# Kernel optimization log

Hardware: AMD Instinct MI355X
Metric: run time of the kernel (lower is better)

## Reference

```python
import jax, jax.numpy as jnp
import numpy as np

S, B, E, H = 512, 64, 512, 512  # seq_len, batch, embed_dim, lstm_dim


def setup_inputs() -> dict:
    key = jax.random.key(0)
    ks = jax.random.split(key, 16)
    scale = 0.03

    def W(k):
        return jax.random.normal(k, (E + H, H), jnp.float32) * scale

    return {
        "embedded_tokens": jax.random.normal(ks[0], (S, B, E), jnp.float32),
        "hidden0": jnp.zeros((B, H), jnp.float32),
        "context0": jnp.zeros((B, H), jnp.float32),
        "Wf": W(ks[1]), "bf": jnp.zeros((H,), jnp.float32),
        "Wi": W(ks[2]), "bi": jnp.zeros((H,), jnp.float32),
        "Wo": W(ks[3]), "bo": jnp.zeros((H,), jnp.float32),
        "Wc": W(ks[4]), "bc": jnp.zeros((H,), jnp.float32),
        "Wmf": W(ks[5]), "bmf": jnp.zeros((H,), jnp.float32),
        "Wmi": W(ks[6]), "bmi": jnp.zeros((H,), jnp.float32),
        "seq_lengths": jax.random.randint(ks[7], (B,), 1, S + 1, jnp.int32),
    }


def reference(embedded_tokens, hidden0, context0, Wf, bf, Wi, bi, Wo, bo,
              Wc, bc, Wmf, bmf, Wmi, bmi, seq_lengths):
    # ON-LSTM recurrence, dropout p=0.0 so dropout is identity.
    def step(carry, x_t):
        h, c = carry                                   # [B,H], [B,H]
        z = jnp.concatenate([x_t, h], axis=1)          # [B, E+H]
        ft = jax.nn.sigmoid(z @ Wf + bf)
        it = jax.nn.sigmoid(z @ Wi + bi)
        ot = jax.nn.sigmoid(z @ Wo + bo)
        c_hat = jnp.tanh(z @ Wc + bc)
        mf = jnp.cumsum(jax.nn.softmax(z @ Wmf + bmf, axis=1), axis=1)  # master forget (cumax)
        mi = jnp.cumsum(jax.nn.softmax(z @ Wmi + bmi, axis=1), axis=1)  # master input (cumax)
        wt = mf * mi
        f_hat = ft * wt + (mf - wt)
        i_hat = it * wt + (mi - wt)
        c = f_hat * c + i_hat * c_hat
        h = ot * c
        return (h, c), (h, c)

    (_h, _c), (all_h, all_c) = jax.lax.scan(step, (hidden0, context0), embedded_tokens)
    # gather final valid state per example
    t_idx = seq_lengths - 1                            # [B]
    b_idx = jnp.arange(all_h.shape[1])
    state_hidden = all_h[t_idx, b_idx]                 # [B,H]
    state_context = all_c[t_idx, b_idx]                # [B,H]
    return all_h, state_hidden, state_context
```

## Files before the change

kernel.cpp:

```cpp
#include <hip/hip_runtime.h>

#define S_LEN 512
#define NWG   64
#define COLS  48
#define OUT_ALLH (512*64*512)
#define OUT_SH   (OUT_ALLH)
#define OUT_SC   (OUT_ALLH + 64*512)

#define O_WT    0ull
#define SZ_WT   (3072ull*1024*2)
#define O_BIAS  (O_WT + SZ_WT)
#define SZ_BIAS (3072ull*4)
#define O_HBF   (O_BIAS + SZ_BIAS)
#define SZ_HBF  (2ull*64*512*2)
#define O_FLAGH (O_HBF + SZ_HBF)
#define O_FLAGP (O_FLAGH + 256)
#define O_P     (O_FLAGP + 256)
#define SZ_P    (64ull*128*4)
#define O_XBF   (O_P + SZ_P)
#define SZ_XBF  (512ull*64*512*2)
#define WS_FULL (O_XBF + SZ_XBF)

#define L_WLDS  0
#define L_PLDS  98304
#define L_GATES 132096
#define L_CST   145664
#define L_BLDS  147968
#define L_SLEN  148160
#define L_PART  148416
#define SMEM_TOTAL 150464

#define GSTR 53
#define PSTR 132

typedef short bf16x8 __attribute__((ext_vector_type(8)));
typedef float f32x4  __attribute__((ext_vector_type(4)));

__device__ __forceinline__ unsigned short f2bf(float f) {
  unsigned u = __float_as_uint(f);
  u += 0x7fffu + ((u >> 16) & 1u);
  return (unsigned short)(u >> 16);
}

#define ATOM_LD(p)    __hip_atomic_load((p), __ATOMIC_RELAXED, __HIP_MEMORY_SCOPE_AGENT)
#define ATOM_ST(p, v) __hip_atomic_store((p), (v), __ATOMIC_RELAXED, __HIP_MEMORY_SCOPE_AGENT)

struct PrepArgs {
  const float* W[6]; const float* bia[6];
  const float* h0;
  unsigned short* WT; float* bias_all; unsigned short* Hbf;
  int* flagH; int* flagP;
};

__global__ void prep_kernel(PrepArgs a) {
  const int n = blockIdx.x, tid = threadIdx.x;
  if (n < 3072) {
    const int q = n >> 9, col = n & 511;
    const float* Wq = a.W[q];
    for (int k = tid; k < 1024; k += 256)
      a.WT[(size_t)n*1024 + k] = f2bf(Wq[k*512 + col]);
    if (tid == 0) a.bias_all[n] = a.bia[q][col];
  } else if (n < 3136) {
    const int r = n - 3072;
    for (int h = tid; h < 512; h += 256) {
      const int w = h >> 3, c = h & 7;
      a.Hbf[(size_t)(64 + w)*512 + r*8 + c] = f2bf(a.h0[r*512 + h]);
    }
  } else {
    if (tid < 64) a.flagH[tid] = 0;
    else if (tid < 128) a.flagP[tid - 64] = 0;
  }
}

__global__ void convx_kernel(const float* __restrict__ x, unsigned short* __restrict__ xbf) {
  const size_t i = ((size_t)blockIdx.x*256 + threadIdx.x) * 4;
  float4 v = *(const float4*)(x + i);
  ushort4 r;
  r.x = f2bf(v.x); r.y = f2bf(v.y); r.z = f2bf(v.z); r.w = f2bf(v.w);
  *(ushort4*)(xbf + i) = r;
}

struct LstmArgs {
  const float* x; const unsigned short* xbf; const float* c0; const int* slen;
  const unsigned short* WT; const float* bias_all; unsigned short* Hbf;
  int* flagH; int* flagP; float* P; float* out;
};

__device__ __forceinline__ void gemm_q(const uint4* af, const char* wlds,
                                       int lane, int kh, f32x4* acc) {
  #pragma unroll
  for (int kt = 0; kt < 8; ++kt) {
    bf16x8 a = *(const bf16x8*)&af[kt];
    #pragma unroll
    for (int nt = 0; nt < 3; ++nt) {
      const int bcol = nt*16 + (lane & 15);
      const int bkc  = kh*32 + kt*4 + (lane >> 4);
      bf16x8 b = *(const bf16x8*)(wlds + bcol*2048 + (((bkc + bcol) & 127) << 4));
      acc[nt] = __builtin_amdgcn_mfma_f32_16x16x32_bf16(a, b, acc[nt], 0, 0, 0);
    }
  }
}

__device__ __forceinline__ void load_xf(const LstmArgs& a, bool ux, int t, int q,
                                        int arow, int lane, uint4 xf[8]) {
  #pragma unroll
  for (int kt = 0; kt < 8; ++kt) {
    const size_t off = ((size_t)t*64 + arow)*512 + (size_t)(q*32 + kt*4 + (lane >> 4))*8;
    if (ux) {
      xf[kt] = *(const uint4*)(a.xbf + off);
    } else {
      const float* sp = a.x + off;
      float4 v0 = *(const float4*)(sp);
      float4 v1 = *(const float4*)(sp + 4);
      xf[kt].x = (unsigned)f2bf(v0.x) | ((unsigned)f2bf(v0.y) << 16);
      xf[kt].y = (unsigned)f2bf(v0.z) | ((unsigned)f2bf(v0.w) << 16);
      xf[kt].z = (unsigned)f2bf(v1.x) | ((unsigned)f2bf(v1.y) << 16);
      xf[kt].w = (unsigned)f2bf(v1.z) | ((unsigned)f2bf(v1.w) << 16);
    }
  }
}

__launch_bounds__(256, 1)
__global__ void lstm_kernel(LstmArgs a) {
  extern __shared__ char smem[];
  char*  wlds  = smem + L_WLDS;
  float* Plds  = (float*)(smem + L_PLDS);
  float* gates = (float*)(smem + L_GATES);
  float* cst   = (float*)(smem + L_CST);
  float* blds  = (float*)(smem + L_BLDS);
  int*   slenl = (int*)(smem + L_SLEN);
  float* part  = (float*)(smem + L_PART);

  const int wg = blockIdx.x, tid = threadIdx.x;
  const int lane = tid & 63, wv = tid >> 6;
  const int arow = wv*16 + (lane & 15);
  const bool ux = (a.xbf != nullptr);

  for (int m = tid; m < COLS*128; m += 256) {
    const int col = m >> 7, kc = m & 127;
    const int q = col >> 3, c = col & 7;
    uint4 v = *(const uint4*)(a.WT + ((size_t)(q*512 + wg*8 + c))*1024 + kc*8);
    *(uint4*)(wlds + col*2048 + (((kc + col) & 127) << 4)) = v;
  }
  if (tid < COLS) { const int q = tid >> 3, c = tid & 7; blds[tid] = a.bias_all[q*512 + wg*8 + c]; }
  if (tid < 64) slenl[tid] = a.slen[tid];
  for (int e = tid; e < 512; e += 256) { const int r = e >> 3, c = e & 7; cst[r*9 + c] = a.c0[r*512 + wg*8 + c]; }
  __syncthreads();

  f32x4 accC[3] = { f32x4{0,0,0,0}, f32x4{0,0,0,0}, f32x4{0,0,0,0} };
  {
    uint4 xf[8];
    load_xf(a, ux, 0, 0, arow, lane, xf);
    gemm_q(xf, wlds, lane, 0, accC);
    load_xf(a, ux, 0, 1, arow, lane, xf);
    gemm_q(xf, wlds, lane, 1, accC);
  }

  for (int t = 0; t < S_LEN; ++t) {
    if (tid < 64) {
      while (ATOM_LD(&a.flagH[tid]) < t)
        __builtin_amdgcn_s_sleep(1);
    }
    __syncthreads();

    const int buf = (t+1) & 1;
    {
      uint4 hf[16];
      #pragma unroll
      for (int j = 0; j < 16; ++j) {
        const int wl = (j & 7)*4 + (lane >> 4) + ((j >> 3) << 5);
        const unsigned short* src = a.Hbf + ((size_t)(buf*64 + wl))*512 + (size_t)arow*8;
        asm volatile("global_load_dwordx4 %0, %1, off sc0 sc1" : "=v"(hf[j]) : "v"(src));
      }
      asm volatile("s_waitcnt vmcnt(8)" ::: "memory");
      __builtin_amdgcn_sched_barrier(0);
      gemm_q(&hf[0], wlds, lane, 2, accC);
      asm volatile("s_waitcnt vmcnt(0)" ::: "memory");
      __builtin_amdgcn_sched_barrier(0);
      gemm_q(&hf[8], wlds, lane, 3, accC);
    }

    #pragma unroll
    for (int nt = 0; nt < 3; ++nt)
      #pragma unroll
      for (int ri = 0; ri < 4; ++ri) {
        const int row = wv*16 + (lane >> 4)*4 + ri;
        gates[row*GSTR + nt*16 + (lane & 15)] = accC[nt][ri];
      }
    __syncthreads();

    const unsigned ep = (unsigned)(t & 1);
    const int tn = t + 1;

    if (tid < 128) {
      const int gi = tid >> 6, r = tid & 63;
      float s = 0.f;
      #pragma unroll
      for (int c = 0; c < 8; ++c) {
        float e = __expf(gates[r*GSTR + (4+gi)*8 + c] + blds[(4+gi)*8 + c]);
        gates[r*GSTR + (4+gi)*8 + c] = e;
        s += e;
      }
      ATOM_ST((unsigned*)(a.P + (size_t)wg*128 + tid), __float_as_uint(s) | (ep << 31));
    }

    f32x4 accN[3] = { f32x4{0,0,0,0}, f32x4{0,0,0,0}, f32x4{0,0,0,0} };
    uint4 xf[8];
    if (tn < S_LEN) {
      load_xf(a, ux, tn, 0, arow, lane, xf);
      gemm_q(xf, wlds, lane, 0, accN);
    }

    #pragma unroll
    for (int j = 0; j < 8; ++j) {
      const int m2 = tid + j*256;
      const int r = m2 >> 5, c = m2 & 31;
      const float v = gates[r*GSTR + c] + blds[c];
      const float e = __expf((c < 24) ? -v : 2.f*v);
      gates[r*GSTR + c] = (c < 24) ? 1.f/(1.f+e) : (e-1.f)/(e+1.f);
    }

    uint4 pbuf[8];
    {
      bool ok = false;
      do {
        #pragma unroll
        for (int j = 0; j < 8; ++j) {
          const int idx = tid + j*256;
          const float* src = a.P + (size_t)idx*4;
          asm volatile("global_load_dwordx4 %0, %1, off sc0 sc1" : "=v"(pbuf[j]) : "v"(src));
        }
        asm volatile("s_waitcnt vmcnt(0)" ::: "memory");
        __builtin_amdgcn_sched_barrier(0);
        unsigned agg = ep ? 0xFFFFFFFFu : 0u;
        #pragma unroll
        for (int j = 0; j < 8; ++j) {
          if (ep) agg &= (pbuf[j].x & pbuf[j].y & pbuf[j].z & pbuf[j].w);
          else    agg |= (pbuf[j].x | pbuf[j].y | pbuf[j].z | pbuf[j].w);
        }
        ok = ((agg >> 31) == ep);
        if (!ok) __builtin_amdgcn_s_sleep(1);
      } while (!ok);
    }

    #pragma unroll
    for (int j = 0; j < 8; ++j) {
      const int idx = tid + j*256;
      const int w = idx >> 5, o = (idx & 31)*4;
      *(uint4*)((char*)Plds + ((size_t)w*PSTR + o)*4) = pbuf[j];
    }
    __syncthreads();

    {
      const int p = tid >> 1, half = tid & 1;
      const int gi = p >> 6, r = p & 63;
      float tot = 0.f, offv = 0.f;
      #pragma unroll
      for (int i = 0; i < 32; ++i) {
        const int w = half*32 + i;
        const float v = __builtin_fabsf(Plds[w*PSTR + gi*64 + r]);
        tot += v;
        if (w < wg) offv += v;
      }
      *(float2*)(part + tid*2) = make_float2(tot, offv);
    }
    __syncthreads();
    if (tid < 128) {
      const int gi = tid >> 6, r = tid & 63;
      float4 pp = *(const float4*)(part + tid*4);
      const float inv = 1.f / (pp.x + pp.z);
      float run = pp.y + pp.w;
      #pragma unroll
      for (int c = 0; c < 8; ++c) {
        run += gates[r*GSTR + (4+gi)*8 + c];
        gates[r*GSTR + (4+gi)*8 + c] = run * inv;
      }
    }
    __syncthreads();

    float hv[2], cv2[2];
    const int er = tid >> 2, ec0 = (tid & 3)*2;
    {
      const float* g = gates + er*GSTR;
      #pragma unroll
      for (int u = 0; u < 2; ++u) {
        const int c = ec0 + u;
        const float ft = g[c];
        const float it = g[8 + c];
        const float ot = g[16 + c];
        const float ch = g[24 + c];
        const float mf = g[32 + c];
        const float mi = g[40 + c];
        const float w2 = mf * mi;
        const float fh = ft * w2 + (mf - w2);
        const float ih = it * w2 + (mi - w2);
        const float cn = fh * cst[er*9 + c] + ih * ch;
        cst[er*9 + c] = cn;
        cv2[u] = cn;
        hv[u] = ot * cn;
      }
      const unsigned pk = (unsigned)f2bf(hv[0]) | ((unsigned)f2bf(hv[1]) << 16);
      ATOM_ST((unsigned*)(a.Hbf + ((size_t)((t & 1)*64 + wg))*512 + er*8 + ec0), pk);
    }
    asm volatile("s_waitcnt vmcnt(0)" ::: "memory");
    __syncthreads();
    if (tid == 0) ATOM_ST(&a.flagH[wg], t+1);

    if (tn < S_LEN) {
      load_xf(a, ux, tn, 1, arow, lane, xf);
      gemm_q(xf, wlds, lane, 1, accN);
    }

    {
      const int col = wg*8 + ec0;
      *(float2*)(a.out + (size_t)t*32768 + er*512 + col) = make_float2(hv[0], hv[1]);
      if (t == slenl[er] - 1) {
        *(float2*)(a.out + (size_t)OUT_SH + er*512 + col) = make_float2(hv[0], hv[1]);
        *(float2*)(a.out + (size_t)OUT_SC + er*512 + col) = make_float2(cv2[0], cv2[1]);
      }
    }

    accC[0] = accN[0]; accC[1] = accN[1]; accC[2] = accN[2];
  }
}

extern "C" void kernel_launch(void* const* d_in, const int* in_sizes, int n_in,
                              void* d_out, int out_size, void* d_ws, size_t ws_size,
                              hipStream_t stream) {
  char* ws = (char*)d_ws;

  PrepArgs pa;
  for (int q = 0; q < 6; ++q) {
    pa.W[q]   = (const float*)d_in[3 + 2*q];
    pa.bia[q] = (const float*)d_in[4 + 2*q];
  }
  pa.h0       = (const float*)d_in[1];
  pa.WT       = (unsigned short*)(ws + O_WT);
  pa.bias_all = (float*)(ws + O_BIAS);
  pa.Hbf      = (unsigned short*)(ws + O_HBF);
  pa.flagH    = (int*)(ws + O_FLAGH);
  pa.flagP    = (int*)(ws + O_FLAGP);
  prep_kernel<<<3137, 256, 0, stream>>>(pa);

  const bool ux = (ws_size >= WS_FULL);
  if (ux)
    convx_kernel<<<16384, 256, 0, stream>>>((const float*)d_in[0], (unsigned short*)(ws + O_XBF));

  LstmArgs la;
  la.x        = (const float*)d_in[0];
  la.xbf      = ux ? (const unsigned short*)(ws + O_XBF) : nullptr;
  la.c0       = (const float*)d_in[2];
  la.slen     = (const int*)d_in[15];
  la.WT       = pa.WT;
  la.bias_all = pa.bias_all;
  la.Hbf      = pa.Hbf;
  la.flagH    = pa.flagH;
  la.flagP    = pa.flagP;
  la.P        = (float*)(ws + O_P);
  la.out      = (float*)d_out;

  hipFuncSetAttribute(reinterpret_cast<const void*>(lstm_kernel),
                      hipFuncAttributeMaxDynamicSharedMemorySize, SMEM_TOTAL);
  lstm_kernel<<<NWG, 256, SMEM_TOTAL, stream>>>(la);
}
```

Before: 4.047 ms.

## Embed step tags in hidden-state words, drop flag barrier, reorder gate GEMMs

Each bf16 hidden pair is now packed into a 64-bit word together with its timestep tag. Consumers poll the data itself until every tag matches, which replaces the separate per-workgroup flag, the store drain and the extra barrier. The hidden-state GEMM is reordered so the master-gate columns are computed first and their softmax partial sums are published early, before the other gate columns. This aims to shorten the per-step cross-workgroup critical path, at the cost of doubling hidden-state traffic and spinning on wider loads; the sleep in the partial-sum poll is also removed.

```diff
diff --git a/kernel.cpp b/kernel.cpp
--- a/kernel.cpp
+++ b/kernel.cpp
@@ -12,10 +12,8 @@
 #define O_BIAS  (O_WT + SZ_WT)
 #define SZ_BIAS (3072ull*4)
 #define O_HBF   (O_BIAS + SZ_BIAS)
-#define SZ_HBF  (2ull*64*512*2)
-#define O_FLAGH (O_HBF + SZ_HBF)
-#define O_FLAGP (O_FLAGH + 256)
-#define O_P     (O_FLAGP + 256)
+#define SZ_HBF  (2ull*64*64*4*8)
+#define O_P     (O_HBF + SZ_HBF)
 #define SZ_P    (64ull*128*4)
 #define O_XBF   (O_P + SZ_P)
 #define SZ_XBF  (512ull*64*512*2)
@@ -48,8 +46,7 @@
 struct PrepArgs {
   const float* W[6]; const float* bia[6];
   const float* h0;
-  unsigned short* WT; float* bias_all; unsigned short* Hbf;
-  int* flagH; int* flagP;
+  unsigned short* WT; float* bias_all; unsigned long long* Hbf;
 };
 
 __global__ void prep_kernel(PrepArgs a) {
@@ -60,15 +57,13 @@
     for (int k = tid; k < 1024; k += 256)
       a.WT[(size_t)n*1024 + k] = f2bf(Wq[k*512 + col]);
     if (tid == 0) a.bias_all[n] = a.bia[q][col];
-  } else if (n < 3136) {
+  } else {
     const int r = n - 3072;
-    for (int h = tid; h < 512; h += 256) {
-      const int w = h >> 3, c = h & 7;
-      a.Hbf[(size_t)(64 + w)*512 + r*8 + c] = f2bf(a.h0[r*512 + h]);
-    }
-  } else {
-    if (tid < 64) a.flagH[tid] = 0;
-    else if (tid < 128) a.flagP[tid - 64] = 0;
+    const int w = tid >> 2, u = tid & 3;
+    const int c0 = w*8 + u*2;
+    const unsigned pk = (unsigned)f2bf(a.h0[r*512 + c0]) |
+                        ((unsigned)f2bf(a.h0[r*512 + c0 + 1]) << 16);
+    a.Hbf[((size_t)(64 + w)*64 + r)*4 + u] = (unsigned long long)pk;
   }
 }
 
@@ -82,22 +77,25 @@
 
 struct LstmArgs {
   const float* x; const unsigned short* xbf; const float* c0; const int* slen;
-  const unsigned short* WT; const float* bias_all; unsigned short* Hbf;
-  int* flagH; int* flagP; float* P; float* out;
+  const unsigned short* WT; const float* bias_all; unsigned long long* Hbf;
+  float* P; float* out;
 };
 
-__device__ __forceinline__ void gemm_q(const uint4* af, const char* wlds,
-                                       int lane, int kh, f32x4* acc) {
+__device__ __forceinline__ void gemm_one(const uint4& afr, const char* wlds,
+                                         int lane, int bkc, int nt, f32x4& acc) {
+  const int bcol = nt*16 + (lane & 15);
+  bf16x8 b = *(const bf16x8*)(wlds + bcol*2048 + (((bkc + bcol) & 127) << 4));
+  bf16x8 av = *(const bf16x8*)&afr;
+  acc = __builtin_amdgcn_mfma_f32_16x16x32_bf16(av, b, acc, 0, 0, 0);
+}
+
+__device__ __forceinline__ void gemm_q3(const uint4* af, const char* wlds,
+                                        int lane, int kh, f32x4* acc) {
   #pragma unroll
   for (int kt = 0; kt < 8; ++kt) {
-    bf16x8 a = *(const bf16x8*)&af[kt];
-    #pragma unroll
-    for (int nt = 0; nt < 3; ++nt) {
-      const int bcol = nt*16 + (lane & 15);
-      const int bkc  = kh*32 + kt*4 + (lane >> 4);
-      bf16x8 b = *(const bf16x8*)(wlds + bcol*2048 + (((bkc + bcol) & 127) << 4));
-      acc[nt] = __builtin_amdgcn_mfma_f32_16x16x32_bf16(a, b, acc[nt], 0, 0, 0);
-    }
+    const int bkc = kh*32 + kt*4 + (lane >> 4);
+    #pragma unroll
+    for (int nt = 0; nt < 3; ++nt) gemm_one(af[kt], wlds, lane, bkc, nt, acc[nt]);
   }
 }
 
@@ -151,65 +149,96 @@
   {
     uint4 xf[8];
     load_xf(a, ux, 0, 0, arow, lane, xf);
-    gemm_q(xf, wlds, lane, 0, accC);
+    gemm_q3(xf, wlds, lane, 0, accC);
     load_xf(a, ux, 0, 1, arow, lane, xf);
-    gemm_q(xf, wlds, lane, 1, accC);
+    gemm_q3(xf, wlds, lane, 1, accC);
   }
 
   for (int t = 0; t < S_LEN; ++t) {
-    if (tid < 64) {
-      while (ATOM_LD(&a.flagH[tid]) < t)
-        __builtin_amdgcn_s_sleep(1);
-    }
-    __syncthreads();
-
     const int buf = (t+1) & 1;
-    {
-      uint4 hf[16];
-      #pragma unroll
-      for (int j = 0; j < 16; ++j) {
-        const int wl = (j & 7)*4 + (lane >> 4) + ((j >> 3) << 5);
-        const unsigned short* src = a.Hbf + ((size_t)(buf*64 + wl))*512 + (size_t)arow*8;
-        asm volatile("global_load_dwordx4 %0, %1, off sc0 sc1" : "=v"(hf[j]) : "v"(src));
-      }
-      asm volatile("s_waitcnt vmcnt(8)" ::: "memory");
-      __builtin_amdgcn_sched_barrier(0);
-      gemm_q(&hf[0], wlds, lane, 2, accC);
-      asm volatile("s_waitcnt vmcnt(0)" ::: "memory");
-      __builtin_amdgcn_sched_barrier(0);
-      gemm_q(&hf[8], wlds, lane, 3, accC);
-    }
-
-    #pragma unroll
-    for (int nt = 0; nt < 3; ++nt)
+    const unsigned expect = (unsigned)t;
+    const unsigned long long* Hq = a.Hbf + (size_t)buf*16384;
+
+    uint4 hf[16];
+    #pragma unroll
+    for (int q = 0; q < 2; ++q) {
+      bool ok;
+      do {
+        uint4 raw[16];
+        #pragma unroll
+        for (int kt = 0; kt < 8; ++kt) {
+          const int c8 = q*32 + kt*4 + (lane >> 4);
+          const unsigned long long* up = Hq + (size_t)c8*256 + (size_t)arow*4;
+          asm volatile("global_load_dwordx4 %0, %1, off sc0 sc1" : "=v"(raw[kt*2])   : "v"(up));
+          asm volatile("global_load_dwordx4 %0, %1, off sc0 sc1" : "=v"(raw[kt*2+1]) : "v"(up+2));
+        }
+        asm volatile("s_waitcnt vmcnt(0)" ::: "memory");
+        __builtin_amdgcn_sched_barrier(0);
+        unsigned diff = 0;
+        #pragma unroll
+        for (int kt = 0; kt < 8; ++kt) {
+          const uint4 r0 = raw[kt*2], r1 = raw[kt*2+1];
+          hf[q*8+kt] = uint4{r0.x, r0.z, r1.x, r1.z};
+          diff |= (r0.y ^ expect) | (r0.w ^ expect) | (r1.y ^ expect) | (r1.w ^ expect);
+        }
+        ok = (diff == 0u);
+        if (!ok) __builtin_amdgcn_s_sleep(1);
+      } while (!ok);
+    }
+
+    #pragma unroll
+    for (int q = 0; q < 2; ++q)
+      #pragma unroll
+      for (int kt = 0; kt < 8; ++kt)
+        gemm_one(hf[q*8+kt], wlds, lane, (2+q)*32 + kt*4 + (lane >> 4), 2, accC[2]);
+
+    #pragma unroll
+    for (int ri = 0; ri < 4; ++ri) {
+      const int row = wv*16 + (lane >> 4)*4 + ri;
+      gates[row*GSTR + 32 + (lane & 15)] = accC[2][ri];
+    }
+    __syncthreads();
+
+    const unsigned ep = (unsigned)(t & 1);
+    const int tn = t + 1;
+
+    if (tid < 128) {
+      const int gi = tid >> 6, r = tid & 63;
+      float s = 0.f;
+      #pragma unroll
+      for (int c = 0; c < 8; ++c) {
+        float e = __expf(gates[r*GSTR + 32 + gi*8 + c] + blds[32 + gi*8 + c]);
+        e = fmaxf(e, 1e-30f);
+        gates[r*GSTR + 32 + gi*8 + c] = e;
+        s += e;
+      }
+      ATOM_ST((unsigned*)(a.P + (size_t)wg*128 + tid), __float_as_uint(s) | (ep << 31));
+    }
+
+    #pragma unroll
+    for (int q = 0; q < 2; ++q)
+      #pragma unroll
+      for (int kt = 0; kt < 8; ++kt) {
+        const int bkc = (2+q)*32 + kt*4 + (lane >> 4);
+        gemm_one(hf[q*8+kt], wlds, lane, bkc, 0, accC[0]);
+        gemm_one(hf[q*8+kt], wlds, lane, bkc, 1, accC[1]);
+      }
+
+    #pragma unroll
+    for (int nt = 0; nt < 2; ++nt)
       #pragma unroll
       for (int ri = 0; ri < 4; ++ri) {
         const int row = wv*16 + (lane >> 4)*4 + ri;
         gates[row*GSTR + nt*16 + (lane & 15)] = accC[nt][ri];
       }
-    __syncthreads();
-
-    const unsigned ep = (unsigned)(t & 1);
-    const int tn = t + 1;
-
-    if (tid < 128) {
-      const int gi = tid >> 6, r = tid & 63;
-      float s = 0.f;
-      #pragma unroll
-      for (int c = 0; c < 8; ++c) {
-        float e = __expf(gates[r*GSTR + (4+gi)*8 + c] + blds[(4+gi)*8 + c]);
-        gates[r*GSTR + (4+gi)*8 + c] = e;
-        s += e;
-      }
-      ATOM_ST((unsigned*)(a.P + (size_t)wg*128 + tid), __float_as_uint(s) | (ep << 31));
-    }
 
     f32x4 accN[3] = { f32x4{0,0,0,0}, f32x4{0,0,0,0}, f32x4{0,0,0,0} };
     uint4 xf[8];
     if (tn < S_LEN) {
       load_xf(a, ux, tn, 0, arow, lane, xf);
-      gemm_q(xf, wlds, lane, 0, accN);
-    }
+      gemm_q3(xf, wlds, lane, 0, accN);
+    }
+    __syncthreads();
 
     #pragma unroll
     for (int j = 0; j < 8; ++j) {
@@ -239,7 +268,6 @@
           else    agg |= (pbuf[j].x | pbuf[j].y | pbuf[j].z | pbuf[j].w);
         }
         ok = ((agg >> 31) == ep);
-        if (!ok) __builtin_amdgcn_s_sleep(1);
       } while (!ok);
     }
 
@@ -272,14 +300,14 @@
       float run = pp.y + pp.w;
       #pragma unroll
       for (int c = 0; c < 8; ++c) {
-        run += gates[r*GSTR + (4+gi)*8 + c];
-        gates[r*GSTR + (4+gi)*8 + c] = run * inv;
+        run += gates[r*GSTR + 32 + gi*8 + c];
+        gates[r*GSTR + 32 + gi*8 + c] = run * inv;
       }
     }
     __syncthreads();
 
     float hv[2], cv2[2];
-    const int er = tid >> 2, ec0 = (tid & 3)*2;
+    const int er = tid >> 2, eu = tid & 3, ec0 = eu*2;
     {
       const float* g = gates + er*GSTR;
       #pragma unroll
@@ -300,15 +328,13 @@
         hv[u] = ot * cn;
       }
       const unsigned pk = (unsigned)f2bf(hv[0]) | ((unsigned)f2bf(hv[1]) << 16);
-      ATOM_ST((unsigned*)(a.Hbf + ((size_t)((t & 1)*64 + wg))*512 + er*8 + ec0), pk);
-    }
-    asm volatile("s_waitcnt vmcnt(0)" ::: "memory");
-    __syncthreads();
-    if (tid == 0) ATOM_ST(&a.flagH[wg], t+1);
+      const unsigned long long val = ((unsigned long long)(unsigned)(t+1) << 32) | (unsigned long long)pk;
+      ATOM_ST(a.Hbf + (size_t)((t & 1)*64 + wg)*256 + (size_t)er*4 + eu, val);
+    }
 
     if (tn < S_LEN) {
       load_xf(a, ux, tn, 1, arow, lane, xf);
-      gemm_q(xf, wlds, lane, 1, accN);
+      gemm_q3(xf, wlds, lane, 1, accN);
     }
 
     {
@@ -337,10 +363,8 @@
   pa.h0       = (const float*)d_in[1];
   pa.WT       = (unsigned short*)(ws + O_WT);
   pa.bias_all = (float*)(ws + O_BIAS);
-  pa.Hbf      = (unsigned short*)(ws + O_HBF);
-  pa.flagH    = (int*)(ws + O_FLAGH);
-  pa.flagP    = (int*)(ws + O_FLAGP);
-  prep_kernel<<<3137, 256, 0, stream>>>(pa);
+  pa.Hbf      = (unsigned long long*)(ws + O_HBF);
+  prep_kernel<<<3136, 256, 0, stream>>>(pa);
 
   const bool ux = (ws_size >= WS_FULL);
   if (ux)
@@ -354,8 +378,6 @@
   la.WT       = pa.WT;
   la.bias_all = pa.bias_all;
   la.Hbf      = pa.Hbf;
-  la.flagH    = pa.flagH;
-  la.flagP    = pa.flagP;
   la.P        = (float*)(ws + O_P);
   la.out      = (float*)d_out;
 
```

New measurement: 4.526 ms. 1.12x slower.

## Compute gates in registers and publish softmax partial sums before the other gate MFMAs

Applied to the files above, without the earlier changes.

The LDS gates staging buffer is removed. Gate activations, softmax exponentials and the cumsum (via lane shuffles) are computed directly from the MFMA accumulators, and lane-pair shuffles combine the gate values for the cell update. The master-gate h-part MFMAs are reordered to run first, so the cross-workgroup softmax partial sums are published to global memory earlier, while the f/i/o/c MFMAs overlap the wait on other workgroups. This removes LDS round trips and a barrier from the serial recurrence critical path. In exchange it adds shuffle work and a small hbuf/cbuf exchange, and clamps exp to 1e-30.

```diff
diff --git a/kernel.cpp b/kernel.cpp
--- a/kernel.cpp
+++ b/kernel.cpp
@@ -14,8 +14,7 @@
 #define O_HBF   (O_BIAS + SZ_BIAS)
 #define SZ_HBF  (2ull*64*512*2)
 #define O_FLAGH (O_HBF + SZ_HBF)
-#define O_FLAGP (O_FLAGH + 256)
-#define O_P     (O_FLAGP + 256)
+#define O_P     (O_FLAGH + 256)
 #define SZ_P    (64ull*128*4)
 #define O_XBF   (O_P + SZ_P)
 #define SZ_XBF  (512ull*64*512*2)
@@ -23,14 +22,13 @@
 
 #define L_WLDS  0
 #define L_PLDS  98304
-#define L_GATES 132096
-#define L_CST   145664
-#define L_BLDS  147968
-#define L_SLEN  148160
-#define L_PART  148416
-#define SMEM_TOTAL 150464
-
-#define GSTR 53
+#define L_PART  132096
+#define L_HBUF  134144
+#define L_CBUF  136192
+#define L_BLDS  138240
+#define L_SLEN  138432
+#define SMEM_TOTAL 138688
+
 #define PSTR 132
 
 typedef short bf16x8 __attribute__((ext_vector_type(8)));
@@ -49,7 +47,7 @@
   const float* W[6]; const float* bia[6];
   const float* h0;
   unsigned short* WT; float* bias_all; unsigned short* Hbf;
-  int* flagH; int* flagP;
+  int* flagH;
 };
 
 __global__ void prep_kernel(PrepArgs a) {
@@ -68,7 +66,6 @@
     }
   } else {
     if (tid < 64) a.flagH[tid] = 0;
-    else if (tid < 128) a.flagP[tid - 64] = 0;
   }
 }
 
@@ -83,21 +80,24 @@
 struct LstmArgs {
   const float* x; const unsigned short* xbf; const float* c0; const int* slen;
   const unsigned short* WT; const float* bias_all; unsigned short* Hbf;
-  int* flagH; int* flagP; float* P; float* out;
+  int* flagH; float* P; float* out;
 };
 
-__device__ __forceinline__ void gemm_q(const uint4* af, const char* wlds,
-                                       int lane, int kh, f32x4* acc) {
+__device__ __forceinline__ void gemm_one(const uint4& afr, const char* wlds,
+                                         int lane, int bkc, int nt, f32x4& acc) {
+  const int bcol = nt*16 + (lane & 15);
+  bf16x8 b = *(const bf16x8*)(wlds + bcol*2048 + (((bkc + bcol) & 127) << 4));
+  bf16x8 av = *(const bf16x8*)&afr;
+  acc = __builtin_amdgcn_mfma_f32_16x16x32_bf16(av, b, acc, 0, 0, 0);
+}
+
+__device__ __forceinline__ void gemm_q3(const uint4* af, const char* wlds,
+                                        int lane, int kh, f32x4* acc) {
   #pragma unroll
   for (int kt = 0; kt < 8; ++kt) {
-    bf16x8 a = *(const bf16x8*)&af[kt];
-    #pragma unroll
-    for (int nt = 0; nt < 3; ++nt) {
-      const int bcol = nt*16 + (lane & 15);
-      const int bkc  = kh*32 + kt*4 + (lane >> 4);
-      bf16x8 b = *(const bf16x8*)(wlds + bcol*2048 + (((bkc + bcol) & 127) << 4));
-      acc[nt] = __builtin_amdgcn_mfma_f32_16x16x32_bf16(a, b, acc[nt], 0, 0, 0);
-    }
+    const int bkc = kh*32 + kt*4 + (lane >> 4);
+    #pragma unroll
+    for (int nt = 0; nt < 3; ++nt) gemm_one(af[kt], wlds, lane, bkc, nt, acc[nt]);
   }
 }
 
@@ -125,35 +125,47 @@
   extern __shared__ char smem[];
   char*  wlds  = smem + L_WLDS;
   float* Plds  = (float*)(smem + L_PLDS);
-  float* gates = (float*)(smem + L_GATES);
-  float* cst   = (float*)(smem + L_CST);
+  float* part  = (float*)(smem + L_PART);
+  float* hbuf  = (float*)(smem + L_HBUF);
+  float* cbuf  = (float*)(smem + L_CBUF);
   float* blds  = (float*)(smem + L_BLDS);
   int*   slenl = (int*)(smem + L_SLEN);
-  float* part  = (float*)(smem + L_PART);
 
   const int wg = blockIdx.x, tid = threadIdx.x;
   const int lane = tid & 63, wv = tid >> 6;
+  const int g = lane >> 4;
+  const int c = lane & 7;
+  const bool hib = (lane & 8) != 0;
   const int arow = wv*16 + (lane & 15);
+  const int crow0 = wv*16 + g*4;
   const bool ux = (a.xbf != nullptr);
 
   for (int m = tid; m < COLS*128; m += 256) {
     const int col = m >> 7, kc = m & 127;
-    const int q = col >> 3, c = col & 7;
-    uint4 v = *(const uint4*)(a.WT + ((size_t)(q*512 + wg*8 + c))*1024 + kc*8);
+    const int q = col >> 3, cc = col & 7;
+    uint4 v = *(const uint4*)(a.WT + ((size_t)(q*512 + wg*8 + cc))*1024 + kc*8);
     *(uint4*)(wlds + col*2048 + (((kc + col) & 127) << 4)) = v;
   }
-  if (tid < COLS) { const int q = tid >> 3, c = tid & 7; blds[tid] = a.bias_all[q*512 + wg*8 + c]; }
+  if (tid < COLS) { const int q = tid >> 3, cc = tid & 7; blds[tid] = a.bias_all[q*512 + wg*8 + cc]; }
   if (tid < 64) slenl[tid] = a.slen[tid];
-  for (int e = tid; e < 512; e += 256) { const int r = e >> 3, c = e & 7; cst[r*9 + c] = a.c0[r*512 + wg*8 + c]; }
   __syncthreads();
+
+  const float b0 = blds[lane & 15];
+  const float b1 = blds[16 + (lane & 15)];
+  const float b2 = blds[32 + (lane & 15)];
+
+  float cstv[4];
+  #pragma unroll
+  for (int ri = 0; ri < 4; ++ri)
+    cstv[ri] = a.c0[(size_t)(crow0 + ri)*512 + wg*8 + c];
 
   f32x4 accC[3] = { f32x4{0,0,0,0}, f32x4{0,0,0,0}, f32x4{0,0,0,0} };
   {
     uint4 xf[8];
     load_xf(a, ux, 0, 0, arow, lane, xf);
-    gemm_q(xf, wlds, lane, 0, accC);
+    gemm_q3(xf, wlds, lane, 0, accC);
     load_xf(a, ux, 0, 1, arow, lane, xf);
-    gemm_q(xf, wlds, lane, 1, accC);
+    gemm_q3(xf, wlds, lane, 1, accC);
   }
 
   for (int t = 0; t < S_LEN; ++t) {
@@ -164,60 +176,75 @@
     __syncthreads();
 
     const int buf = (t+1) & 1;
-    {
-      uint4 hf[16];
-      #pragma unroll
-      for (int j = 0; j < 16; ++j) {
-        const int wl = (j & 7)*4 + (lane >> 4) + ((j >> 3) << 5);
-        const unsigned short* src = a.Hbf + ((size_t)(buf*64 + wl))*512 + (size_t)arow*8;
-        asm volatile("global_load_dwordx4 %0, %1, off sc0 sc1" : "=v"(hf[j]) : "v"(src));
-      }
-      asm volatile("s_waitcnt vmcnt(8)" ::: "memory");
-      __builtin_amdgcn_sched_barrier(0);
-      gemm_q(&hf[0], wlds, lane, 2, accC);
-      asm volatile("s_waitcnt vmcnt(0)" ::: "memory");
-      __builtin_amdgcn_sched_barrier(0);
-      gemm_q(&hf[8], wlds, lane, 3, accC);
-    }
-
-    #pragma unroll
-    for (int nt = 0; nt < 3; ++nt)
-      #pragma unroll
-      for (int ri = 0; ri < 4; ++ri) {
-        const int row = wv*16 + (lane >> 4)*4 + ri;
-        gates[row*GSTR + nt*16 + (lane & 15)] = accC[nt][ri];
-      }
-    __syncthreads();
+    uint4 hf[16];
+    #pragma unroll
+    for (int j = 0; j < 16; ++j) {
+      const int wl = (j & 7)*4 + (lane >> 4) + ((j >> 3) << 5);
+      const unsigned short* src = a.Hbf + ((size_t)(buf*64 + wl))*512 + (size_t)arow*8;
+      asm volatile("global_load_dwordx4 %0, %1, off sc0 sc1" : "=v"(hf[j]) : "v"(src));
+    }
+    f32x4 acc2b = f32x4{0,0,0,0};
+    asm volatile("s_waitcnt vmcnt(8)" ::: "memory");
+    __builtin_amdgcn_sched_barrier(0);
+    #pragma unroll
+    for (int kt = 0; kt < 8; ++kt)
+      gemm_one(hf[kt], wlds, lane, 2*32 + kt*4 + (lane >> 4), 2, accC[2]);
+    asm volatile("s_waitcnt vmcnt(0)" ::: "memory");
+    __builtin_amdgcn_sched_barrier(0);
+    #pragma unroll
+    for (int kt = 0; kt < 8; ++kt)
+      gemm_one(hf[8+kt], wlds, lane, 3*32 + kt*4 + (lane >> 4), 2, acc2b);
 
     const unsigned ep = (unsigned)(t & 1);
     const int tn = t + 1;
 
-    if (tid < 128) {
-      const int gi = tid >> 6, r = tid & 63;
-      float s = 0.f;
-      #pragma unroll
-      for (int c = 0; c < 8; ++c) {
-        float e = __expf(gates[r*GSTR + (4+gi)*8 + c] + blds[(4+gi)*8 + c]);
-        gates[r*GSTR + (4+gi)*8 + c] = e;
-        s += e;
+    float e4[4], s4[4];
+    #pragma unroll
+    for (int ri = 0; ri < 4; ++ri) {
+      float e = __expf(accC[2][ri] + acc2b[ri] + b2);
+      e = fmaxf(e, 1e-30f);
+      e4[ri] = e; s4[ri] = e;
+    }
+    #pragma unroll
+    for (int m = 1; m < 8; m <<= 1)
+      #pragma unroll
+      for (int ri = 0; ri < 4; ++ri)
+        s4[ri] += __shfl_xor(s4[ri], m, 64);
+    if ((lane & 7) == 0) {
+      const int base = wg*128 + (hib ? 64 : 0) + crow0;
+      const unsigned u0 = __float_as_uint(s4[0]) | (ep << 31);
+      const unsigned u1 = __float_as_uint(s4[1]) | (ep << 31);
+      const unsigned u2 = __float_as_uint(s4[2]) | (ep << 31);
+      const unsigned u3 = __float_as_uint(s4[3]) | (ep << 31);
+      ATOM_ST((unsigned long long*)(a.P + base),     ((unsigned long long)u1 << 32) | u0);
+      ATOM_ST((unsigned long long*)(a.P + base + 2), ((unsigned long long)u3 << 32) | u2);
+    }
+
+    #pragma unroll
+    for (int q = 0; q < 2; ++q)
+      #pragma unroll
+      for (int kt = 0; kt < 8; ++kt) {
+        const int bkc = (2+q)*32 + kt*4 + (lane >> 4);
+        gemm_one(hf[q*8+kt], wlds, lane, bkc, 0, accC[0]);
+        gemm_one(hf[q*8+kt], wlds, lane, bkc, 1, accC[1]);
       }
-      ATOM_ST((unsigned*)(a.P + (size_t)wg*128 + tid), __float_as_uint(s) | (ep << 31));
-    }
 
     f32x4 accN[3] = { f32x4{0,0,0,0}, f32x4{0,0,0,0}, f32x4{0,0,0,0} };
     uint4 xf[8];
     if (tn < S_LEN) {
       load_xf(a, ux, tn, 0, arow, lane, xf);
-      gemm_q(xf, wlds, lane, 0, accN);
-    }
-
-    #pragma unroll
-    for (int j = 0; j < 8; ++j) {
-      const int m2 = tid + j*256;
-      const int r = m2 >> 5, c = m2 & 31;
-      const float v = gates[r*GSTR + c] + blds[c];
-      const float e = __expf((c < 24) ? -v : 2.f*v);
-      gates[r*GSTR + c] = (c < 24) ? 1.f/(1.f+e) : (e-1.f)/(e+1.f);
+      gemm_q3(xf, wlds, lane, 0, accN);
+    }
+
+    float t0[4], t1[4];
+    #pragma unroll
+    for (int ri = 0; ri < 4; ++ri) {
+      const float v0 = accC[0][ri] + b0;
+      t0[ri] = __builtin_amdgcn_rcpf(1.f + __expf(-v0));
+      const float v1 = accC[1][ri] + b1;
+      const float e = __expf(hib ? 2.f*v1 : -v1);
+      const float r = __builtin_amdgcn_rcpf(1.f + e);
+      t1[ri] = hib ? (e - 1.f)*r : r;
     }
 
     uint4 pbuf[8];
@@ -253,54 +280,71 @@
 
     {
       const int p = tid >> 1, half = tid & 1;
-      const int gi = p >> 6, r = p & 63;
       float tot = 0.f, offv = 0.f;
       #pragma unroll
       for (int i = 0; i < 32; ++i) {
         const int w = half*32 + i;
-        const float v = __builtin_fabsf(Plds[w*PSTR + gi*64 + r]);
+        const float v = __builtin_fabsf(Plds[w*PSTR + p]);
         tot += v;
         if (w < wg) offv += v;
       }
       *(float2*)(part + tid*2) = make_float2(tot, offv);
     }
     __syncthreads();
-    if (tid < 128) {
-      const int gi = tid >> 6, r = tid & 63;
-      float4 pp = *(const float4*)(part + tid*4);
-      const float inv = 1.f / (pp.x + pp.z);
-      float run = pp.y + pp.w;
-      #pragma unroll
-      for (int c = 0; c < 8; ++c) {
-        run += gates[r*GSTR + (4+gi)*8 + c];
-        gates[r*GSTR + (4+gi)*8 + c] = run * inv;
+
+    float m4[4];
+    {
+      float pr[4];
+      #pragma unroll
+      for (int ri = 0; ri < 4; ++ri) pr[ri] = e4[ri];
+      #pragma unroll
+      for (int d = 1; d < 8; d <<= 1)
+        #pragma unroll
+        for (int ri = 0; ri < 4; ++ri) {
+          const float v = __shfl_up(pr[ri], d, 8);
+          if (c >= d) pr[ri] += v;
+        }
+      #pragma unroll
+      for (int ri = 0; ri < 4; ++ri) {
+        const int p = (hib ? 64 : 0) + crow0 + ri;
+        const float4 pp = *(const float4*)(part + p*4);
+        const float inv = __builtin_amdgcn_rcpf(pp.x + pp.z);
+        m4[ri] = ((pp.y + pp.w) + pr[ri]) * inv;
       }
     }
+
+    float hv4[4], cn4[4];
+    #pragma unroll
+    for (int ri = 0; ri < 4; ++ri) {
+      const float q0 = __shfl_xor(t0[ri], 8, 64);
+      const float q1 = __shfl_xor(t1[ri], 8, 64);
+      const float qm = __shfl_xor(m4[ri], 8, 64);
+      const float f  = hib ? q0 : t0[ri];
+      const float i_ = hib ? t0[ri] : q0;
+      const float o  = hib ? q1 : t1[ri];
+      const float ch = hib ? t1[ri] : q1;
+      const float mf = hib ? qm : m4[ri];
+      const float mi = hib ? m4[ri] : qm;
+      const float w2 = mf * mi;
+      const float cn = (f*w2 + (mf - w2))*cstv[ri] + (i_*w2 + (mi - w2))*ch;
+      cstv[ri] = cn;
+      cn4[ri] = cn;
+      hv4[ri] = o * cn;
+    }
+    if (!hib) {
+      #pragma unroll
+      for (int ri = 0; ri < 4; ++ri) {
+        hbuf[(crow0 + ri)*8 + c] = hv4[ri];
+        cbuf[(crow0 + ri)*8 + c] = cn4[ri];
+      }
+    }
     __syncthreads();
 
-    float hv[2], cv2[2];
-    const int er = tid >> 2, ec0 = (tid & 3)*2;
+    const int er = tid >> 2, eu = tid & 3;
+    const float h0 = hbuf[er*8 + eu*2], h1 = hbuf[er*8 + eu*2 + 1];
     {
-      const float* g = gates + er*GSTR;
-      #pragma unroll
-      for (int u = 0; u < 2; ++u) {
-        const int c = ec0 + u;
-        const float ft = g[c];
-        const float it = g[8 + c];
-        const float ot = g[16 + c];
-        const float ch = g[24 + c];
-        const float mf = g[32 + c];
-        const float mi = g[40 + c];
-        const float w2 = mf * mi;
-        const float fh = ft * w2 + (mf - w2);
-        const float ih = it * w2 + (mi - w2);
-        const float cn = fh * cst[er*9 + c] + ih * ch;
-        cst[er*9 + c] = cn;
-        cv2[u] = cn;
-        hv[u] = ot * cn;
-      }
-      const unsigned pk = (unsigned)f2bf(hv[0]) | ((unsigned)f2bf(hv[1]) << 16);
-      ATOM_ST((unsigned*)(a.Hbf + ((size_t)((t & 1)*64 + wg))*512 + er*8 + ec0), pk);
+      const unsigned pk = (unsigned)f2bf(h0) | ((unsigned)f2bf(h1) << 16);
+      ATOM_ST((unsigned*)(a.Hbf + ((size_t)((t & 1)*64 + wg))*512 + er*8 + eu*2), pk);
     }
     asm volatile("s_waitcnt vmcnt(0)" ::: "memory");
     __syncthreads();
@@ -308,15 +352,16 @@
 
     if (tn < S_LEN) {
       load_xf(a, ux, tn, 1, arow, lane, xf);
-      gemm_q(xf, wlds, lane, 1, accN);
+      gemm_q3(xf, wlds, lane, 1, accN);
     }
 
     {
-      const int col = wg*8 + ec0;
-      *(float2*)(a.out + (size_t)t*32768 + er*512 + col) = make_float2(hv[0], hv[1]);
+      const int col = wg*8 + eu*2;
+      *(float2*)(a.out + (size_t)t*32768 + er*512 + col) = make_float2(h0, h1);
       if (t == slenl[er] - 1) {
-        *(float2*)(a.out + (size_t)OUT_SH + er*512 + col) = make_float2(hv[0], hv[1]);
-        *(float2*)(a.out + (size_t)OUT_SC + er*512 + col) = make_float2(cv2[0], cv2[1]);
+        *(float2*)(a.out + (size_t)OUT_SH + er*512 + col) = make_float2(h0, h1);
+        *(float2*)(a.out + (size_t)OUT_SC + er*512 + col) =
+            make_float2(cbuf[er*8 + eu*2], cbuf[er*8 + eu*2 + 1]);
       }
     }
 
@@ -339,7 +384,6 @@
   pa.bias_all = (float*)(ws + O_BIAS);
   pa.Hbf      = (unsigned short*)(ws + O_HBF);
   pa.flagH    = (int*)(ws + O_FLAGH);
-  pa.flagP    = (int*)(ws + O_FLAGP);
   prep_kernel<<<3137, 256, 0, stream>>>(pa);
 
   const bool ux = (ws_size >= WS_FULL);
@@ -355,7 +399,6 @@
   la.bias_all = pa.bias_all;
   la.Hbf      = pa.Hbf;
   la.flagH    = pa.flagH;
-  la.flagP    = pa.flagP;
   la.P        = (float*)(ws + O_P);
   la.out      = (float*)d_out;
 
```

New measurement: 4.382 ms. +8.3%, slower.
